# Kernel tuning notes

Hardware: AMD Instinct MI355X
Metric: run time of the kernel (lower is better)

The kernel has to match this reference:

```python
import jax, jax.numpy as jnp
import numpy as np

WINDOW_SIZE = 11
CHANNEL = 3
DATA_RANGE = 1.0
C1 = (0.01 * DATA_RANGE) ** 2
C2 = (0.03 * DATA_RANGE) ** 2


def _gaussian_window(window_size, channel, sigma=1.5):
    coords = np.arange(window_size, dtype=np.float32) - window_size // 2
    g = np.exp(-coords ** 2 / (2 * sigma ** 2))
    g = g / g.sum()
    g2d = g[:, None] * g[None, :]  # [K, K]
    # depthwise conv weight in OIHW with groups=channel -> [C, 1, K, K]
    w = np.broadcast_to(g2d[None, None], (channel, 1, window_size, window_size))
    return jnp.asarray(np.ascontiguousarray(w))


def _dwconv(x, w):
    # depthwise conv, stride 1, SAME padding (== pad window//2 for odd kernel)
    return jax.lax.conv_general_dilated(
        x, w, window_strides=(1, 1), padding='SAME',
        feature_group_count=x.shape[1],
        dimension_numbers=('NCHW', 'OIHW', 'NCHW'))


def setup_inputs() -> dict:
    key = jax.random.key(0)
    k1, k2 = jax.random.split(key)
    img1 = jax.random.normal(k1, (32, 3, 512, 512), dtype=jnp.float32)
    img2 = jax.random.normal(k2, (32, 3, 512, 512), dtype=jnp.float32)
    window = _gaussian_window(WINDOW_SIZE, CHANNEL)
    return {"img1": img1, "img2": img2, "window": window}


def reference(img1, img2, window):
    mu1 = _dwconv(img1, window)
    mu2 = _dwconv(img2, window)
    mu1_sq = mu1 * mu1
    mu2_sq = mu2 * mu2
    mu1_mu2 = mu1 * mu2
    sigma1_sq = jnp.maximum(_dwconv(img1 * img1, window) - mu1_sq, 0.0)
    sigma2_sq = jnp.maximum(_dwconv(img2 * img2, window) - mu2_sq, 0.0)
    sigma12 = _dwconv(img1 * img2, window) - mu1_mu2
    s1 = jnp.sqrt(sigma1_sq)
    s2 = jnp.sqrt(sigma2_sq)
    luminance = (2.0 * mu1_mu2 + C1) / (mu1_sq + mu2_sq + C1)
    contrast = (2.0 * s1 * s2 + C2) / (sigma1_sq + sigma2_sq + C2)
    structure = (sigma12 + C2 / 2) / (s1 * s2 + C2 / 2)
    ssim_map = luminance * contrast * structure
    return jnp.mean(ssim_map)
```

## Files before the change

### kernel.cpp

```cpp
#include <hip/hip_runtime.h>
#include <stdint.h>


#define IMG_H 512
#define IMG_W 512
#define WAVE_W 64
#define STRIPE 128
#define HALO 5
#define KW 11
#define N_ROWT (IMG_H / STRIPE)
#define N_COLT (IMG_W / WAVE_W)
#define N_TILES (96 * N_ROWT * N_COLT)
#define WPB 4
#define N_BLOCKS (N_TILES / WPB)
#define T_MAX 143
#define NBINS 256
#define TOTAL_PIX (32.0f * 3.0f * 512.0f * 512.0f)

__global__ __launch_bounds__(64 * WPB)
void ssim_main(
    const float* __restrict__ img1, const float* __restrict__ img2,
    const float* __restrict__ window, float* __restrict__ bins)
{
    __shared__ float buf_all[WPB][4][2][128];
    __shared__ float dump_all[WPB][64];

    const int lane = threadIdx.x & 63;
    const int wv   = threadIdx.x >> 6;
    float (* __restrict__ buf)[2][128] = buf_all[wv];
    float* __restrict__ dump = dump_all[wv];

    float g[KW];
    {
        const float inv = rsqrtf(window[5*KW + 5]);
        #pragma unroll
        for (int k = 0; k < KW; ++k)
            g[k] = __int_as_float(
                __builtin_amdgcn_readfirstlane(
                    __float_as_int(window[5*KW + k] * inv)));
    }

    const int b   = blockIdx.x * WPB + wv;
    const int img = b >> 5;
    const int rem = b & 31;
    const int ty  = rem >> 3;
    const int tx  = rem & 7;
    const int r0  = ty * STRIPE;
    const int x0  = tx * WAVE_W;

    const float* __restrict__ p1 = img1 + (size_t)img * (IMG_H * IMG_W);
    const float* __restrict__ p2 = img2 + (size_t)img * (IMG_H * IMG_W);

    const int cm = min(max(x0 - HALO + lane, 0), IMG_W - 1);
    const int ct = min(max(x0 + WAVE_W - HALO + lane, 0), IMG_W - 1);

    const float* pm1 = p1 + (long)(r0 - HALO) * IMG_W + cm;
    const float* pm2 = p2 + (long)(r0 - HALO) * IMG_W + cm;
    const float* pt1 = p1 + (long)(r0 - HALO) * IMG_W + ct;
    const float* pt2 = p2 + (long)(r0 - HALO) * IMG_W + ct;
    const float* pdm = p1 + lane;

    auto issue = [&](int tl) {
        const int slot = tl & 3;
        float* s0 = &buf[slot][0][0];
        float* s1 = &buf[slot][1][0];
        if ((unsigned)(r0 - HALO + tl) < IMG_H) {
            __builtin_amdgcn_global_load_lds(pm1, s0,      4, 0, 0);
            __builtin_amdgcn_global_load_lds(pt1, s0 + 64, 4, 0, 0);
            __builtin_amdgcn_global_load_lds(pm2, s1,      4, 0, 0);
            __builtin_amdgcn_global_load_lds(pt2, s1 + 64, 4, 0, 0);
        } else {
            __builtin_amdgcn_global_load_lds(pdm, dump, 4, 0, 0);
            __builtin_amdgcn_global_load_lds(pdm, dump, 4, 0, 0);
            __builtin_amdgcn_global_load_lds(pdm, dump, 4, 0, 0);
            __builtin_amdgcn_global_load_lds(pdm, dump, 4, 0, 0);
            s0[lane] = 0.f; s0[64 + lane] = 0.f;
            s1[lane] = 0.f; s1[64 + lane] = 0.f;
        }
        pm1 += IMG_W; pm2 += IMG_W; pt1 += IMG_W; pt2 += IMG_W;
    };

    float r_h1[KW], r_h2[KW], r_h11[KW], r_h22[KW], r_h12[KW];
    #pragma unroll
    for (int i = 0; i < KW; ++i) {
        r_h1[i] = 0.f; r_h2[i] = 0.f; r_h11[i] = 0.f; r_h22[i] = 0.f; r_h12[i] = 0.f;
    }

    const float C1 = 1e-4f;
    const float C2 = 9e-4f;
    float sum = 0.f;

    issue(0); issue(1); issue(2);

    #pragma unroll 1
    for (int tb = 0; tb < T_MAX; tb += KW) {
        #pragma unroll
        for (int u = 0; u < KW; ++u) {
            const int t = tb + u;

            issue(t + 3);

            asm volatile("s_waitcnt vmcnt(12)" ::: "memory");

            if (tx == 0) {
                if (lane < HALO) {
                    buf[t & 3][0][lane] = 0.f;
                    buf[t & 3][1][lane] = 0.f;
                }
            }
            if (tx == 7) {
                if (lane >= HALO && lane < 2*HALO) {
                    buf[t & 3][0][64 + lane] = 0.f;
                    buf[t & 3][1][64 + lane] = 0.f;
                }
            }

            const float* bA = &buf[t & 3][0][lane];
            const float* bB = &buf[t & 3][1][lane];
            float h1 = 0.f, h2 = 0.f, h11 = 0.f, h22 = 0.f, h12 = 0.f;
            #pragma unroll
            for (int k = 0; k < KW; ++k) {
                const float va = bA[k];
                const float vb = bB[k];
                const float t1 = g[k] * va;
                const float t2 = g[k] * vb;
                h1  += t1;
                h2  += t2;
                h11 += t1 * va;
                h22 += t2 * vb;
                h12 += t1 * vb;
            }
            asm volatile("" ::: "memory");

            r_h1[u] = h1; r_h2[u] = h2; r_h11[u] = h11; r_h22[u] = h22; r_h12[u] = h12;

            if (t >= 2*HALO && t < 2*HALO + STRIPE) {
                float mu1 = 0.f, mu2 = 0.f, e11 = 0.f, e22 = 0.f, e12 = 0.f;
                #pragma unroll
                for (int m = 0; m < KW; ++m) {
                    const int slot = (u + 1 + m) % KW;
                    mu1 += g[m] * r_h1[slot];
                    mu2 += g[m] * r_h2[slot];
                    e11 += g[m] * r_h11[slot];
                    e22 += g[m] * r_h22[slot];
                    e12 += g[m] * r_h12[slot];
                }
                const float mu1s = mu1 * mu1, mu2s = mu2 * mu2, mu12 = mu1 * mu2;
                const float s1  = fmaxf(e11 - mu1s, 0.f);
                const float s2  = fmaxf(e22 - mu2s, 0.f);
                const float s12 = e12 - mu12;
                const float num = (2.f * mu12 + C1) * (2.f * s12 + C2);
                const float den = (mu1s + mu2s + C1) * (s1 + s2 + C2);
                sum += num * __builtin_amdgcn_rcpf(den);
            }
        }
    }

    asm volatile("s_waitcnt vmcnt(0)" ::: "memory");

    #pragma unroll
    for (int off = 32; off > 0; off >>= 1)
        sum += __shfl_down(sum, off, 64);
    if (lane == 0)
        atomicAdd(&bins[b & (NBINS - 1)], sum);
}

__global__ __launch_bounds__(64) void ssim_final(
    const float* __restrict__ bins, float* __restrict__ out)
{
    const int tid = threadIdx.x;
    float s = 0.f;
    #pragma unroll
    for (int i = 0; i < NBINS / 64; ++i) s += bins[tid + i * 64];
    #pragma unroll
    for (int off = 32; off > 0; off >>= 1)
        s += __shfl_down(s, off, 64);
    if (tid == 0) out[0] = s * (1.0f / TOTAL_PIX);
}

extern "C" void kernel_launch(void* const* d_in, const int* in_sizes, int n_in,
                              void* d_out, int out_size, void* d_ws, size_t ws_size,
                              hipStream_t stream) {
    const float* img1   = (const float*)d_in[0];
    const float* img2   = (const float*)d_in[1];
    const float* window = (const float*)d_in[2];
    float* bins = (float*)d_ws;
    float* out  = (float*)d_out;

    hipMemsetAsync(bins, 0, NBINS * sizeof(float), stream);
    ssim_main<<<N_BLOCKS, 64 * WPB, 0, stream>>>(img1, img2, window, bins);
    ssim_final<<<1, 64, 0, stream>>>(bins, out);
}
```

Baseline: 329.9 us.

## Process rows in pairs with packed float2 math and deeper 6-slot LDS pipeline

Restructures the row loop to handle two rows per step. The row ring grows to 12 entries and the LDS prefetch ring from 4 to 6 slots, keeping more loads in flight. Horizontal and vertical convolutions now use float2 vectors for the two images so the compiler can emit packed FP32 ops. The loop trip count is fixed exactly to the 138 needed rows with a peeled prologue and epilogue, so no wasted iterations remain. In exchange, register pressure rises and the unrolled code is larger.

Result: faster. 320.6 us (-2.8%).

```diff
diff --git a/kernel.cpp b/kernel.cpp
--- a/kernel.cpp
+++ b/kernel.cpp
@@ -1,6 +1,7 @@
 #include <hip/hip_runtime.h>
-#include <stdint.h>
-
+
+
+typedef float f2 __attribute__((ext_vector_type(2)));
 
 #define IMG_H 512
 #define IMG_W 512
@@ -13,7 +14,7 @@
 #define N_TILES (96 * N_ROWT * N_COLT)
 #define WPB 4
 #define N_BLOCKS (N_TILES / WPB)
-#define T_MAX 143
+#define T_ROWS (STRIPE + 2*HALO)
 #define NBINS 256
 #define TOTAL_PIX (32.0f * 3.0f * 512.0f * 512.0f)
 
@@ -22,7 +23,7 @@
     const float* __restrict__ img1, const float* __restrict__ img2,
     const float* __restrict__ window, float* __restrict__ bins)
 {
-    __shared__ float buf_all[WPB][4][2][128];
+    __shared__ float buf_all[WPB][6][2][128];
     __shared__ float dump_all[WPB][64];
 
     const int lane = threadIdx.x & 63;
@@ -60,101 +61,118 @@
     const float* pt2 = p2 + (long)(r0 - HALO) * IMG_W + ct;
     const float* pdm = p1 + lane;
 
-    auto issue = [&](int tl) {
-        const int slot = tl & 3;
-        float* s0 = &buf[slot][0][0];
-        float* s1 = &buf[slot][1][0];
-        if ((unsigned)(r0 - HALO + tl) < IMG_H) {
-            __builtin_amdgcn_global_load_lds(pm1, s0,      4, 0, 0);
-            __builtin_amdgcn_global_load_lds(pt1, s0 + 64, 4, 0, 0);
-            __builtin_amdgcn_global_load_lds(pm2, s1,      4, 0, 0);
-            __builtin_amdgcn_global_load_lds(pt2, s1 + 64, 4, 0, 0);
-        } else {
-            __builtin_amdgcn_global_load_lds(pdm, dump, 4, 0, 0);
-            __builtin_amdgcn_global_load_lds(pdm, dump, 4, 0, 0);
-            __builtin_amdgcn_global_load_lds(pdm, dump, 4, 0, 0);
-            __builtin_amdgcn_global_load_lds(pdm, dump, 4, 0, 0);
-            s0[lane] = 0.f; s0[64 + lane] = 0.f;
-            s1[lane] = 0.f; s1[64 + lane] = 0.f;
-        }
-        pm1 += IMG_W; pm2 += IMG_W; pt1 += IMG_W; pt2 += IMG_W;
-    };
-
-    float r_h1[KW], r_h2[KW], r_h11[KW], r_h22[KW], r_h12[KW];
-    #pragma unroll
-    for (int i = 0; i < KW; ++i) {
-        r_h1[i] = 0.f; r_h2[i] = 0.f; r_h11[i] = 0.f; r_h22[i] = 0.f; r_h12[i] = 0.f;
+    const bool fixL = (tx == 0)        && (lane < HALO);
+    const bool fixR = (tx == N_COLT-1) && (lane >= HALO && lane < 2*HALO);
+
+    f2 rab[12], rsq[12];
+    float rx[12];
+    #pragma unroll
+    for (int i = 0; i < 12; ++i) {
+        rab[i] = (f2){0.f, 0.f}; rsq[i] = (f2){0.f, 0.f}; rx[i] = 0.f;
     }
 
-    const float C1 = 1e-4f;
-    const float C2 = 9e-4f;
+    const float C1 = 1e-4f, C2 = 9e-4f;
     float sum = 0.f;
 
-    issue(0); issue(1); issue(2);
+#define ISSUE(SLOT, TL) do {                                                  \
+        float* s0_ = &buf[(SLOT)][0][0];                                      \
+        float* s1_ = &buf[(SLOT)][1][0];                                      \
+        const int gy_ = r0 - HALO + (TL);                                     \
+        if ((TL) < T_ROWS && (unsigned)gy_ < IMG_H) {                         \
+            __builtin_amdgcn_global_load_lds(pm1, s0_,      4, 0, 0);         \
+            __builtin_amdgcn_global_load_lds(pt1, s0_ + 64, 4, 0, 0);         \
+            __builtin_amdgcn_global_load_lds(pm2, s1_,      4, 0, 0);         \
+            __builtin_amdgcn_global_load_lds(pt2, s1_ + 64, 4, 0, 0);         \
+        } else {                                                              \
+            __builtin_amdgcn_global_load_lds(pdm, dump, 4, 0, 0);             \
+            __builtin_amdgcn_global_load_lds(pdm, dump, 4, 0, 0);             \
+            __builtin_amdgcn_global_load_lds(pdm, dump, 4, 0, 0);             \
+            __builtin_amdgcn_global_load_lds(pdm, dump, 4, 0, 0);             \
+            s0_[lane] = 0.f; s0_[64 + lane] = 0.f;                            \
+            s1_[lane] = 0.f; s1_[64 + lane] = 0.f;                            \
+        }                                                                     \
+        pm1 += IMG_W; pm2 += IMG_W; pt1 += IMG_W; pt2 += IMG_W;               \
+    } while (0)
+
+#define HCONV(LSLOT, HS) do {                                                 \
+        const float* bA_ = &buf[(LSLOT)][0][lane];                            \
+        const float* bB_ = &buf[(LSLOT)][1][lane];                            \
+        f2 hab_ = (f2){0.f, 0.f}, hsq_ = (f2){0.f, 0.f};                      \
+        float hx_ = 0.f;                                                      \
+        _Pragma("unroll")                                                     \
+        for (int k = 0; k < KW; ++k) {                                        \
+            f2 v_; v_.x = bA_[k]; v_.y = bB_[k];                              \
+            const f2 t_ = v_ * g[k];                                          \
+            hab_ += t_;                                                       \
+            hsq_ += t_ * v_;                                                  \
+            hx_  = fmaf(t_.x, v_.y, hx_);                                     \
+        }                                                                     \
+        rab[(HS)] = hab_; rsq[(HS)] = hsq_; rx[(HS)] = hx_;                   \
+    } while (0)
+
+#define OUTROW(OFF) do {                                                      \
+        f2 mu_ = (f2){0.f, 0.f}, e_ = (f2){0.f, 0.f};                         \
+        float e12_ = 0.f;                                                     \
+        _Pragma("unroll")                                                     \
+        for (int m = 0; m < KW; ++m) {                                        \
+            const int s_ = ((OFF) + m) % 12;                \
+            mu_ += rab[s_] * g[m];                                            \
+            e_  += rsq[s_] * g[m];                                            \
+            e12_ = fmaf(g[m], rx[s_], e12_);                                  \
+        }                                                                     \
+        const float mu1s_ = mu_.x * mu_.x;                                    \
+        const float mu2s_ = mu_.y * mu_.y;                                    \
+        const float mu12_ = mu_.x * mu_.y;                                    \
+        const float s1_  = fmaxf(e_.x - mu1s_, 0.f);                          \
+        const float s2_  = fmaxf(e_.y - mu2s_, 0.f);                          \
+        const float s12_ = e12_ - mu12_;                                      \
+        const float num_ = (2.f * mu12_ + C1) * (2.f * s12_ + C2);            \
+        const float den_ = (mu1s_ + mu2s_ + C1) * (s1_ + s2_ + C2);           \
+        sum += num_ * __builtin_amdgcn_rcpf(den_);                            \
+    } while (0)
+
+#define PAIR(J, TB, DOGAT) do {                                               \
+        const int t_ = (TB) + 2*(J);                                          \
+        ISSUE((2*(J)+4) % 6, t_ + 4);                                         \
+        ISSUE((2*(J)+5) % 6, t_ + 5);                                         \
+           \
+        asm volatile("s_waitcnt vmcnt(16)" ::: "memory");                     \
+        if (fixL) {                                                           \
+            buf[(2*(J))%6][0][lane] = 0.f;   buf[(2*(J))%6][1][lane] = 0.f;   \
+            buf[(2*(J)+1)%6][0][lane] = 0.f; buf[(2*(J)+1)%6][1][lane] = 0.f; \
+        }                                                                     \
+        if (fixR) {                                                           \
+            buf[(2*(J))%6][0][64+lane] = 0.f;   buf[(2*(J))%6][1][64+lane] = 0.f;   \
+            buf[(2*(J)+1)%6][0][64+lane] = 0.f; buf[(2*(J)+1)%6][1][64+lane] = 0.f; \
+        }                                                                     \
+        HCONV((2*(J))%6,   2*(J));                                            \
+        HCONV((2*(J)+1)%6, 2*(J)+1);                                          \
+             \
+        asm volatile("" ::: "memory");                                        \
+        if (DOGAT) {                                                          \
+            OUTROW(2*(J) + 2);                           \
+            OUTROW(2*(J) + 3);                           \
+        }                                                                     \
+    } while (0)
+
+    ISSUE(0, 0); ISSUE(1, 1); ISSUE(2, 2); ISSUE(3, 3);
+
+    PAIR(0, 0, 0); PAIR(1, 0, 0); PAIR(2, 0, 0);
+    PAIR(3, 0, 0); PAIR(4, 0, 0); PAIR(5, 0, 1);
 
     #pragma unroll 1
-    for (int tb = 0; tb < T_MAX; tb += KW) {
+    for (int tb = 12; tb < 132; tb += 12) {
         #pragma unroll
-        for (int u = 0; u < KW; ++u) {
-            const int t = tb + u;
-
-            issue(t + 3);
-
-            asm volatile("s_waitcnt vmcnt(12)" ::: "memory");
-
-            if (tx == 0) {
-                if (lane < HALO) {
-                    buf[t & 3][0][lane] = 0.f;
-                    buf[t & 3][1][lane] = 0.f;
-                }
-            }
-            if (tx == 7) {
-                if (lane >= HALO && lane < 2*HALO) {
-                    buf[t & 3][0][64 + lane] = 0.f;
-                    buf[t & 3][1][64 + lane] = 0.f;
-                }
-            }
-
-            const float* bA = &buf[t & 3][0][lane];
-            const float* bB = &buf[t & 3][1][lane];
-            float h1 = 0.f, h2 = 0.f, h11 = 0.f, h22 = 0.f, h12 = 0.f;
-            #pragma unroll
-            for (int k = 0; k < KW; ++k) {
-                const float va = bA[k];
-                const float vb = bB[k];
-                const float t1 = g[k] * va;
-                const float t2 = g[k] * vb;
-                h1  += t1;
-                h2  += t2;
-                h11 += t1 * va;
-                h22 += t2 * vb;
-                h12 += t1 * vb;
-            }
-            asm volatile("" ::: "memory");
-
-            r_h1[u] = h1; r_h2[u] = h2; r_h11[u] = h11; r_h22[u] = h22; r_h12[u] = h12;
-
-            if (t >= 2*HALO && t < 2*HALO + STRIPE) {
-                float mu1 = 0.f, mu2 = 0.f, e11 = 0.f, e22 = 0.f, e12 = 0.f;
-                #pragma unroll
-                for (int m = 0; m < KW; ++m) {
-                    const int slot = (u + 1 + m) % KW;
-                    mu1 += g[m] * r_h1[slot];
-                    mu2 += g[m] * r_h2[slot];
-                    e11 += g[m] * r_h11[slot];
-                    e22 += g[m] * r_h22[slot];
-                    e12 += g[m] * r_h12[slot];
-                }
-                const float mu1s = mu1 * mu1, mu2s = mu2 * mu2, mu12 = mu1 * mu2;
-                const float s1  = fmaxf(e11 - mu1s, 0.f);
-                const float s2  = fmaxf(e22 - mu2s, 0.f);
-                const float s12 = e12 - mu12;
-                const float num = (2.f * mu12 + C1) * (2.f * s12 + C2);
-                const float den = (mu1s + mu2s + C1) * (s1 + s2 + C2);
-                sum += num * __builtin_amdgcn_rcpf(den);
-            }
-        }
+        for (int j = 0; j < 6; ++j)
+            PAIR(j, tb, 1);
     }
+
+    PAIR(0, 132, 1); PAIR(1, 132, 1); PAIR(2, 132, 1);
+
+#undef PAIR
+#undef OUTROW
+#undef HCONV
+#undef ISSUE
 
     asm volatile("s_waitcnt vmcnt(0)" ::: "memory");
 
```
